# Kernel optimization log

Hardware: AMD Instinct MI355X
Metric: run time of the kernel (lower is better)

Reference implementation:

```python
import jax, jax.numpy as jnp
import numpy as np

EMBED_DIM = 4096
NQ = 32           # query heads
NKV = 8           # kv heads
HEAD = 128        # head dim
KV_SEQ = 4096
B = 8
T = 32
START_POS = 4064  # end_pos = 4096
SCALE = 1.0 / np.sqrt(HEAD)
THETA = 10000.0


def _rope(x, table_len):
    """Faithful replication of the torch module's RoPE, including its bug:
    the torch code unpacks (B,H,T,D)=x.shape on a (B,T_seq,H,D) tensor, so the
    frequency table (of length table_len) is sliced to the first H (=num heads)
    rows and broadcast along the HEAD axis, not the sequence axis.
    x: (B, T_seq, H, D) float32.
    """
    Bn, Tn, H, D = x.shape
    dh = D // 2
    inv_freq = 1.0 / (THETA ** (jnp.arange(dh, dtype=jnp.float32) / dh))  # (dh,)
    pos = jnp.arange(table_len, dtype=jnp.float32)
    freqs = (pos[:, None] * inv_freq[None, :])[:H]  # (H, dh) -- head-indexed!
    cos = jnp.cos(freqs)[None, None]  # (1,1,H,dh)
    sin = jnp.sin(freqs)[None, None]
    xr, xi = x[..., 0::2], x[..., 1::2]  # complex pairs are consecutive elems
    yr = xr * cos - xi * sin
    yi = xr * sin + xi * cos
    return jnp.stack([yr, yi], axis=-1).reshape(Bn, Tn, H, D)


def setup_inputs() -> dict:
    key = jax.random.key(0)
    ks = jax.random.split(key, 5)
    x = jax.random.normal(ks[0], (B, T, EMBED_DIM), dtype=jnp.float32)
    Wq = jax.random.normal(ks[1], (EMBED_DIM, EMBED_DIM), dtype=jnp.float32) * 0.02
    Wk = jax.random.normal(ks[2], (NKV * HEAD, EMBED_DIM), dtype=jnp.float32) * 0.02
    Wv = jax.random.normal(ks[3], (NKV * HEAD, EMBED_DIM), dtype=jnp.float32) * 0.02
    Wo = jax.random.normal(ks[4], (EMBED_DIM, EMBED_DIM), dtype=jnp.float32) * 0.02
    cache_keys = jnp.zeros((B, KV_SEQ * 2, NKV, HEAD), dtype=jnp.float32)
    cache_values = jnp.zeros((B, KV_SEQ * 2, NKV, HEAD), dtype=jnp.float32)
    return {"x": x, "start_pos": START_POS, "cache_keys": cache_keys,
            "cache_values": cache_values, "Wq": Wq, "Wk": Wk, "Wv": Wv, "Wo": Wo}


def reference(x, start_pos, cache_keys, cache_values, Wq, Wk, Wv, Wo):
    Bn, Tn, C = x.shape
    q = (x @ Wq.T).reshape(Bn, Tn, NQ, HEAD)
    k = (x @ Wk.T).reshape(Bn, Tn, NKV, HEAD)
    v = (x @ Wv.T).reshape(Bn, Tn, NKV, HEAD)
    # rope=True branch: q table built for Tn positions, k table for KV_SEQ
    q = _rope(q, Tn)
    k = _rope(k, KV_SEQ)
    end = start_pos + Tn
    # cache write (torch detaches k/v before writing and reads detached views)
    ck = cache_keys.at[:Bn, start_pos:end].set(jax.lax.stop_gradient(k))
    cv = cache_values.at[:Bn, start_pos:end].set(jax.lax.stop_gradient(v))
    k_full = jax.lax.stop_gradient(ck[:Bn, :end])  # (B, end, NKV, D)
    v_full = jax.lax.stop_gradient(cv[:Bn, :end])
    r = NQ // NKV
    kf = jnp.repeat(k_full.transpose(0, 2, 1, 3), r, axis=1)  # (B, NQ, end, D)
    vf = jnp.repeat(v_full.transpose(0, 2, 1, 3), r, axis=1)
    qh = q.transpose(0, 2, 1, 3)                               # (B, NQ, T, D)
    att = jnp.einsum('bhtd,bhsd->bhts', qh, kf) * SCALE        # (B, NQ, T, end)
    causal = jnp.triu(jnp.ones((end, end), dtype=bool), 1)[-Tn:]  # (T, end)
    att = jnp.where(causal[None, None], -jnp.inf, att)
    att = jax.nn.softmax(att, axis=-1)
    out = jnp.einsum('bhts,bhsd->bhtd', att, vf)
    out = out.transpose(0, 2, 1, 3).reshape(Bn, Tn, C)
    return out @ Wo.T
```

## Files before the change

kernel.cpp:

```cpp
#include <hip/hip_runtime.h>
#include <stdint.h>

#define Bb 8
#define Tt 32
#define Ee 4096
#define NQ 32
#define NKV 8
#define HD 128
#define CACHE_S 8192
#define SSPLIT 8
#define SCALE_F 0.08838834764831845f

typedef _Float16 half8 __attribute__((ext_vector_type(8)));
typedef _Float16 half4 __attribute__((ext_vector_type(4)));
typedef float f32x4 __attribute__((ext_vector_type(4)));

static __device__ __forceinline__ _Float16 f2h(float f) { return (_Float16)f; }

__global__ __launch_bounds__(256) void gemm_nt_sk(
    const float* __restrict__ A, const float* __restrict__ W0,
    const float* __restrict__ W1, const float* __restrict__ W2,
    int nsplit1, int nsplit2, float* __restrict__ Cpart, size_t part_stride,
    int K, int Kc, int ldc) {
  __shared__ _Float16 As[64][72];
  __shared__ _Float16 Ws[64][72];
  const int n0 = blockIdx.x * 64;
  const int m0 = blockIdx.y * 64;
  const int kp = blockIdx.z;
  const int kbase = kp * Kc;
  const float* Wp;
  int nr0;
  if (n0 < nsplit1) { Wp = W0; nr0 = n0; }
  else if (n0 < nsplit2) { Wp = W1; nr0 = n0 - nsplit1; }
  else { Wp = W2; nr0 = n0 - nsplit2; }
  const int tid = threadIdx.x;
  const int lane = tid & 63;
  const int wave = tid >> 6;
  const int wm = (wave >> 1) * 32;
  const int wn = (wave & 1) * 32;
  const int l15 = lane & 15;
  const int quad = lane >> 4;
  const int sr = tid >> 4;
  const int sc = (tid & 15) * 4;

  f32x4 acc[2][2];
#pragma unroll
  for (int i = 0; i < 2; i++)
#pragma unroll
    for (int j = 0; j < 2; j++) acc[i][j] = f32x4{0.f, 0.f, 0.f, 0.f};

  float4 pa[4], pw[4];
#pragma unroll
  for (int p = 0; p < 4; p++) {
    const int r = sr + p * 16;
    pa[p] = *(const float4*)&A[(size_t)(m0 + r) * K + kbase + sc];
    pw[p] = *(const float4*)&Wp[(size_t)(nr0 + r) * K + kbase + sc];
  }

  for (int k0 = 0; k0 < Kc; k0 += 64) {
    __syncthreads();
#pragma unroll
    for (int p = 0; p < 4; p++) {
      const int r = sr + p * 16;
      half4 ha = {f2h(pa[p].x), f2h(pa[p].y), f2h(pa[p].z), f2h(pa[p].w)};
      *(half4*)&As[r][sc] = ha;
      half4 hw = {f2h(pw[p].x), f2h(pw[p].y), f2h(pw[p].z), f2h(pw[p].w)};
      *(half4*)&Ws[r][sc] = hw;
    }
    __syncthreads();
    if (k0 + 64 < Kc) {
#pragma unroll
      for (int p = 0; p < 4; p++) {
        const int r = sr + p * 16;
        pa[p] = *(const float4*)&A[(size_t)(m0 + r) * K + kbase + k0 + 64 + sc];
        pw[p] = *(const float4*)&Wp[(size_t)(nr0 + r) * K + kbase + k0 + 64 + sc];
      }
    }
#pragma unroll
    for (int ks = 0; ks < 2; ks++) {
      const int kc = ks * 32 + quad * 8;
      half8 af[2], wf[2];
#pragma unroll
      for (int i = 0; i < 2; i++) {
        af[i] = *(const half8*)&As[wm + i * 16 + l15][kc];
        wf[i] = *(const half8*)&Ws[wn + i * 16 + l15][kc];
      }
#pragma unroll
      for (int i = 0; i < 2; i++)
#pragma unroll
        for (int j = 0; j < 2; j++)
          acc[i][j] = __builtin_amdgcn_mfma_f32_16x16x32_f16(af[i], wf[j],
                                                             acc[i][j], 0, 0, 0);
    }
  }
  float* Cp = Cpart + (size_t)kp * part_stride;
#pragma unroll
  for (int i = 0; i < 2; i++) {
    const int mr = m0 + wm + i * 16 + quad * 4;
#pragma unroll
    for (int j = 0; j < 2; j++) {
      const int nc = n0 + wn + j * 16 + l15;
#pragma unroll
      for (int r = 0; r < 4; r++)
        Cp[(size_t)(mr + r) * ldc + nc] = acc[i][j][r];
    }
  }
}

__global__ __launch_bounds__(256) void rope_scatter(
    const float* __restrict__ qkvp, float* __restrict__ qw,
    float* __restrict__ kw, float* __restrict__ vw) {
  const int pid = blockIdx.x * 256 + threadIdx.x;
  const int m = pid / 3072;
  const int c = pid - m * 3072;
  const int n = c * 2;
  const int b = m >> 5;
  const int t = m & 31;
  const size_t base = (size_t)m * 6144 + n;
  float a0 = 0.f, a1 = 0.f;
#pragma unroll
  for (int p = 0; p < 4; p++) {
    const float2 v = *(const float2*)&qkvp[p * 1572864 + base];
    a0 += v.x;
    a1 += v.y;
  }
  if (n < 4096) {
    const int h = n >> 7;
    const int j = (n & 127) >> 1;
    const float invf = powf(10000.0f, -(float)j * (1.0f / 64.0f));
    float sn, cs;
    sincosf((float)h * invf, &sn, &cs);
    float* dst = qw + ((size_t)(b * NQ + h) * Tt + t) * HD + (j << 1);
    dst[0] = a0 * cs - a1 * sn;
    dst[1] = a0 * sn + a1 * cs;
  } else if (n < 5120) {
    const int nn = n - 4096;
    const int h = nn >> 7;
    const int j = (nn & 127) >> 1;
    const float invf = powf(10000.0f, -(float)j * (1.0f / 64.0f));
    float sn, cs;
    sincosf((float)h * invf, &sn, &cs);
    float* dst = kw + ((size_t)(b * NKV + h) * Tt + t) * HD + (j << 1);
    dst[0] = a0 * cs - a1 * sn;
    dst[1] = a0 * sn + a1 * cs;
  } else {
    const int nn = n - 5120;
    const int h = nn >> 7;
    const int d = nn & 127;
    float* dst = vw + ((size_t)(b * NKV + h) * Tt + t) * HD + d;
    dst[0] = a0;
    dst[1] = a1;
  }
}

__global__ __launch_bounds__(256) void attn_partial(
    const float* __restrict__ qw, const float* __restrict__ kw,
    const float* __restrict__ vw, const float* __restrict__ cacheK,
    const float* __restrict__ cacheV, const int* __restrict__ startp,
    float* __restrict__ pO, float* __restrict__ pM, float* __restrict__ pL) {
  const int blk = blockIdx.x;
  const int split = blk & (SSPLIT - 1);
  const int g = (blk / SSPLIT) & (NKV - 1);
  const int b = blk / (SSPLIT * NKV);
  const int start = *startp;
  const int end = start + Tt;
  int cl = ((end + SSPLIT * 32 - 1) / (SSPLIT * 32)) * 32;
  const int s_begin = split * cl;
  int s_end = s_begin + cl;
  if (s_end > end) s_end = end;

  const int tid = threadIdx.x;
  const int lane = tid & 63;
  const int wave = tid >> 6;
  const int l15 = lane & 15;
  const int quad = lane >> 4;
  const int h = g * 4 + wave;

  __shared__ _Float16 Ks[32][136];
  __shared__ _Float16 Vt[128][40];
  __shared__ _Float16 Ps[4][32][40];

  half8 qf[2][4];
#pragma unroll
  for (int mt = 0; mt < 2; mt++) {
    const int t = mt * 16 + l15;
    const float* qrow = qw + ((size_t)(b * NQ + h) * Tt + t) * HD;
#pragma unroll
    for (int ks = 0; ks < 4; ks++) {
      const int d0 = ks * 32 + quad * 8;
      float4 v0 = *(const float4*)&qrow[d0];
      float4 v1 = *(const float4*)&qrow[d0 + 4];
      half8 hq = {f2h(v0.x), f2h(v0.y), f2h(v0.z), f2h(v0.w),
                  f2h(v1.x), f2h(v1.y), f2h(v1.z), f2h(v1.w)};
      qf[mt][ks] = hq;
    }
  }

  f32x4 Oacc[2][8];
#pragma unroll
  for (int mt = 0; mt < 2; mt++)
#pragma unroll
    for (int dt = 0; dt < 8; dt++) Oacc[mt][dt] = f32x4{0.f, 0.f, 0.f, 0.f};
  float mrow[2][4], lrow[2][4];
#pragma unroll
  for (int mt = 0; mt < 2; mt++)
#pragma unroll
    for (int rr = 0; rr < 4; rr++) { mrow[mt][rr] = -1e30f; lrow[mt][rr] = 0.f; }

  const int str = tid >> 3;
  const int stc = (tid & 7) * 4;

  float4 pk[4], pv[4];
  auto load_chunk = [&](int s0) {
    const int sg = s0 + str;
    const bool valid = sg < end;
    const float* krow;
    const float* vrow;
    if (sg < start) {
      const size_t off = (((size_t)b * CACHE_S + sg) * NKV + g) * HD;
      krow = cacheK + off;
      vrow = cacheV + off;
    } else {
      int loc = sg - start;
      if (loc > Tt - 1) loc = Tt - 1;
      const size_t off = ((size_t)(b * NKV + g) * Tt + loc) * HD;
      krow = kw + off;
      vrow = vw + off;
    }
#pragma unroll
    for (int u = 0; u < 4; u++) {
      const int cc = stc + u * 32;
      pk[u] = valid ? *(const float4*)&krow[cc] : make_float4(0.f, 0.f, 0.f, 0.f);
      pv[u] = valid ? *(const float4*)&vrow[cc] : make_float4(0.f, 0.f, 0.f, 0.f);
    }
  };

  load_chunk(s_begin);

  for (int s0 = s_begin; s0 < s_end; s0 += 32) {
    __syncthreads();
#pragma unroll
    for (int u = 0; u < 4; u++) {
      const int cc = stc + u * 32;
      half4 hk = {f2h(pk[u].x), f2h(pk[u].y), f2h(pk[u].z), f2h(pk[u].w)};
      *(half4*)&Ks[str][cc] = hk;
      Vt[cc + 0][str] = f2h(pv[u].x);
      Vt[cc + 1][str] = f2h(pv[u].y);
      Vt[cc + 2][str] = f2h(pv[u].z);
      Vt[cc + 3][str] = f2h(pv[u].w);
    }
    __syncthreads();
    if (s0 + 32 < s_end) load_chunk(s0 + 32);

    f32x4 st[2][2];
#pragma unroll
    for (int mt = 0; mt < 2; mt++)
#pragma unroll
      for (int nt = 0; nt < 2; nt++) st[mt][nt] = f32x4{0.f, 0.f, 0.f, 0.f};
#pragma unroll
    for (int nt = 0; nt < 2; nt++) {
#pragma unroll
      for (int ks = 0; ks < 4; ks++) {
        half8 kf = *(const half8*)&Ks[nt * 16 + l15][ks * 32 + quad * 8];
        st[0][nt] = __builtin_amdgcn_mfma_f32_16x16x32_f16(qf[0][ks], kf, st[0][nt], 0, 0, 0);
        st[1][nt] = __builtin_amdgcn_mfma_f32_16x16x32_f16(qf[1][ks], kf, st[1][nt], 0, 0, 0);
      }
    }
#pragma unroll
    for (int mt = 0; mt < 2; mt++)
#pragma unroll
      for (int nt = 0; nt < 2; nt++)
#pragma unroll
        for (int rr = 0; rr < 4; rr++) {
          const int t = mt * 16 + quad * 4 + rr;
          const int sg = s0 + nt * 16 + l15;
          const float sv = st[mt][nt][rr] * SCALE_F;
          const bool masked = (sg > start + t) || (sg >= end);
          st[mt][nt][rr] = masked ? -1e30f : sv;
        }
#pragma unroll
    for (int mt = 0; mt < 2; mt++) {
      float rmax[4], rsum[4], al[4];
#pragma unroll
      for (int rr = 0; rr < 4; rr++)
        rmax[rr] = fmaxf(st[mt][0][rr], st[mt][1][rr]);
      for (int mm = 1; mm < 16; mm <<= 1)
#pragma unroll
        for (int rr = 0; rr < 4; rr++)
          rmax[rr] = fmaxf(rmax[rr], __shfl_xor(rmax[rr], mm));
#pragma unroll
      for (int rr = 0; rr < 4; rr++) {
        const float mn = fmaxf(mrow[mt][rr], rmax[rr]);
        al[rr] = __expf(mrow[mt][rr] - mn);
        mrow[mt][rr] = mn;
      }
#pragma unroll
      for (int nt = 0; nt < 2; nt++)
#pragma unroll
        for (int rr = 0; rr < 4; rr++)
          st[mt][nt][rr] = __expf(st[mt][nt][rr] - mrow[mt][rr]);
#pragma unroll
      for (int rr = 0; rr < 4; rr++) rsum[rr] = st[mt][0][rr] + st[mt][1][rr];
      for (int mm = 1; mm < 16; mm <<= 1)
#pragma unroll
        for (int rr = 0; rr < 4; rr++) rsum[rr] += __shfl_xor(rsum[rr], mm);
#pragma unroll
      for (int rr = 0; rr < 4; rr++)
        lrow[mt][rr] = lrow[mt][rr] * al[rr] + rsum[rr];
#pragma unroll
      for (int nt = 0; nt < 2; nt++)
#pragma unroll
        for (int rr = 0; rr < 4; rr++)
          Ps[wave][mt * 16 + quad * 4 + rr][nt * 16 + l15] = f2h(st[mt][nt][rr]);
#pragma unroll
      for (int dt = 0; dt < 8; dt++)
#pragma unroll
        for (int rr = 0; rr < 4; rr++) Oacc[mt][dt][rr] *= al[rr];
    }
    half8 pf0 = *(const half8*)&Ps[wave][l15][quad * 8];
    half8 pf1 = *(const half8*)&Ps[wave][16 + l15][quad * 8];
#pragma unroll
    for (int dt = 0; dt < 8; dt++) {
      half8 vf = *(const half8*)&Vt[dt * 16 + l15][quad * 8];
      Oacc[0][dt] = __builtin_amdgcn_mfma_f32_16x16x32_f16(pf0, vf, Oacc[0][dt], 0, 0, 0);
      Oacc[1][dt] = __builtin_amdgcn_mfma_f32_16x16x32_f16(pf1, vf, Oacc[1][dt], 0, 0, 0);
    }
  }

  const size_t rowbase = (size_t)(b * NQ + h) * Tt;
#pragma unroll
  for (int mt = 0; mt < 2; mt++)
#pragma unroll
    for (int rr = 0; rr < 4; rr++) {
      const int t = mt * 16 + quad * 4 + rr;
      const size_t pbase = ((rowbase + t) * SSPLIT + split) * (size_t)HD;
#pragma unroll
      for (int dt = 0; dt < 8; dt++)
        pO[pbase + dt * 16 + l15] = Oacc[mt][dt][rr];
      if (l15 == 0) {
        pM[(rowbase + t) * SSPLIT + split] = mrow[mt][rr];
        pL[(rowbase + t) * SSPLIT + split] = lrow[mt][rr];
      }
    }
}

__global__ __launch_bounds__(128) void attn_combine(
    const float* __restrict__ pO, const float* __restrict__ pM,
    const float* __restrict__ pL, float* __restrict__ att) {
  const int row = blockIdx.x;
  const int d = threadIdx.x;
  float m[SSPLIT], l[SSPLIT];
  float ms = -3.0e30f;
#pragma unroll
  for (int i = 0; i < SSPLIT; i++) {
    m[i] = pM[row * SSPLIT + i];
    l[i] = pL[row * SSPLIT + i];
    ms = fmaxf(ms, m[i]);
  }
  float ls = 0.f, o = 0.f;
#pragma unroll
  for (int i = 0; i < SSPLIT; i++) {
    const float w = __expf(m[i] - ms);
    ls += l[i] * w;
    o += pO[((size_t)row * SSPLIT + i) * HD + d] * w;
  }
  o /= fmaxf(ls, 1e-30f);
  const int b = row / (NQ * Tt);
  const int hh = (row / Tt) % NQ;
  const int t = row % Tt;
  att[((size_t)(b * Tt + t)) * Ee + hh * HD + d] = o;
}

__global__ __launch_bounds__(256) void reduce2(const float* __restrict__ p0,
                                               const float* __restrict__ p1,
                                               float* __restrict__ out) {
  const int i = (blockIdx.x * 256 + threadIdx.x) * 4;
  float4 a = *(const float4*)&p0[i];
  float4 b = *(const float4*)&p1[i];
  float4 r = make_float4(a.x + b.x, a.y + b.y, a.z + b.z, a.w + b.w);
  *(float4*)&out[i] = r;
}

extern "C" void kernel_launch(void* const* d_in, const int* in_sizes, int n_in,
                              void* d_out, int out_size, void* d_ws,
                              size_t ws_size, hipStream_t stream) {
  const float* x = (const float*)d_in[0];
  const int* startp = (const int*)d_in[1];
  const float* cacheK = (const float*)d_in[2];
  const float* cacheV = (const float*)d_in[3];
  const float* Wq = (const float*)d_in[4];
  const float* Wk = (const float*)d_in[5];
  const float* Wv = (const float*)d_in[6];
  const float* Wo = (const float*)d_in[7];
  float* out = (float*)d_out;
  float* ws = (float*)d_ws;

  float* qkvp = ws;
  float* pO = qkvp + 6291456;
  float* qw = pO + 8388608;
  float* kw = qw + 1048576;
  float* vw = kw + 262144;
  float* pM = vw + 262144;
  float* pL = pM + 65536;
  float* att = pL + 65536;
  float* woP = att + 1048576;

  const dim3 blk(256);
  gemm_nt_sk<<<dim3(96, 4, 4), blk, 0, stream>>>(
      x, Wq, Wk, Wv, 4096, 5120, qkvp, (size_t)256 * 6144, 4096, 1024, 6144);
  rope_scatter<<<dim3(3072), blk, 0, stream>>>(qkvp, qw, kw, vw);
  attn_partial<<<dim3(Bb * NKV * SSPLIT), blk, 0, stream>>>(
      qw, kw, vw, cacheK, cacheV, startp, pO, pM, pL);
  attn_combine<<<dim3(Bb * NQ * Tt), dim3(128), 0, stream>>>(pO, pM, pL, att);
  gemm_nt_sk<<<dim3(64, 4, 2), blk, 0, stream>>>(
      att, Wo, Wo, Wo, 4096, 4096, woP, (size_t)256 * 4096, 4096, 2048, 4096);
  reduce2<<<dim3(1024), blk, 0, stream>>>(woP, woP + 1048576, out);
}
```

Measured before the change: 652.9 us.

## Double-buffer KV chunk prefetch in attention and split Wo GEMM K four ways

The attention partial kernel now keeps two register buffers of K/V data, so loads for chunks two steps ahead are issued before the current chunk is computed. The Q fragment load is moved after the first prefetches so they overlap. This is meant to hide global-memory latency, at the cost of more registers. Separately, the output projection GEMM now splits K four ways instead of two, giving 1024 blocks for better CU occupancy, and a reduce4 kernel sums the four partials, which adds partial-buffer traffic.

```diff
diff --git a/kernel.cpp b/kernel.cpp
--- a/kernel.cpp
+++ b/kernel.cpp
@@ -180,38 +180,11 @@
   __shared__ _Float16 Vt[128][40];
   __shared__ _Float16 Ps[4][32][40];
 
-  half8 qf[2][4];
-#pragma unroll
-  for (int mt = 0; mt < 2; mt++) {
-    const int t = mt * 16 + l15;
-    const float* qrow = qw + ((size_t)(b * NQ + h) * Tt + t) * HD;
-#pragma unroll
-    for (int ks = 0; ks < 4; ks++) {
-      const int d0 = ks * 32 + quad * 8;
-      float4 v0 = *(const float4*)&qrow[d0];
-      float4 v1 = *(const float4*)&qrow[d0 + 4];
-      half8 hq = {f2h(v0.x), f2h(v0.y), f2h(v0.z), f2h(v0.w),
-                  f2h(v1.x), f2h(v1.y), f2h(v1.z), f2h(v1.w)};
-      qf[mt][ks] = hq;
-    }
-  }
-
-  f32x4 Oacc[2][8];
-#pragma unroll
-  for (int mt = 0; mt < 2; mt++)
-#pragma unroll
-    for (int dt = 0; dt < 8; dt++) Oacc[mt][dt] = f32x4{0.f, 0.f, 0.f, 0.f};
-  float mrow[2][4], lrow[2][4];
-#pragma unroll
-  for (int mt = 0; mt < 2; mt++)
-#pragma unroll
-    for (int rr = 0; rr < 4; rr++) { mrow[mt][rr] = -1e30f; lrow[mt][rr] = 0.f; }
-
   const int str = tid >> 3;
   const int stc = (tid & 7) * 4;
 
-  float4 pk[4], pv[4];
-  auto load_chunk = [&](int s0) {
+  float4 pkA[4], pvA[4], pkB[4], pvB[4];
+  auto load_chunk = [&](int s0, float4* pk, float4* pv) {
     const int sg = s0 + str;
     const bool valid = sg < end;
     const float* krow;
@@ -234,11 +207,7 @@
       pv[u] = valid ? *(const float4*)&vrow[cc] : make_float4(0.f, 0.f, 0.f, 0.f);
     }
   };
-
-  load_chunk(s_begin);
-
-  for (int s0 = s_begin; s0 < s_end; s0 += 32) {
-    __syncthreads();
+  auto commit_chunk = [&](const float4* pk, const float4* pv) {
 #pragma unroll
     for (int u = 0; u < 4; u++) {
       const int cc = stc + u * 32;
@@ -249,9 +218,39 @@
       Vt[cc + 2][str] = f2h(pv[u].z);
       Vt[cc + 3][str] = f2h(pv[u].w);
     }
-    __syncthreads();
-    if (s0 + 32 < s_end) load_chunk(s0 + 32);
-
+  };
+
+  load_chunk(s_begin, pkA, pvA);
+  if (s_begin + 32 < s_end) load_chunk(s_begin + 32, pkB, pvB);
+
+  half8 qf[2][4];
+#pragma unroll
+  for (int mt = 0; mt < 2; mt++) {
+    const int t = mt * 16 + l15;
+    const float* qrow = qw + ((size_t)(b * NQ + h) * Tt + t) * HD;
+#pragma unroll
+    for (int ks = 0; ks < 4; ks++) {
+      const int d0 = ks * 32 + quad * 8;
+      float4 v0 = *(const float4*)&qrow[d0];
+      float4 v1 = *(const float4*)&qrow[d0 + 4];
+      half8 hq = {f2h(v0.x), f2h(v0.y), f2h(v0.z), f2h(v0.w),
+                  f2h(v1.x), f2h(v1.y), f2h(v1.z), f2h(v1.w)};
+      qf[mt][ks] = hq;
+    }
+  }
+
+  f32x4 Oacc[2][8];
+#pragma unroll
+  for (int mt = 0; mt < 2; mt++)
+#pragma unroll
+    for (int dt = 0; dt < 8; dt++) Oacc[mt][dt] = f32x4{0.f, 0.f, 0.f, 0.f};
+  float mrow[2][4], lrow[2][4];
+#pragma unroll
+  for (int mt = 0; mt < 2; mt++)
+#pragma unroll
+    for (int rr = 0; rr < 4; rr++) { mrow[mt][rr] = -1e30f; lrow[mt][rr] = 0.f; }
+
+  auto compute_chunk = [&](int s0) {
     f32x4 st[2][2];
 #pragma unroll
     for (int mt = 0; mt < 2; mt++)
@@ -325,6 +324,21 @@
       Oacc[0][dt] = __builtin_amdgcn_mfma_f32_16x16x32_f16(pf0, vf, Oacc[0][dt], 0, 0, 0);
       Oacc[1][dt] = __builtin_amdgcn_mfma_f32_16x16x32_f16(pf1, vf, Oacc[1][dt], 0, 0, 0);
     }
+  };
+
+  for (int s0 = s_begin; s0 < s_end; s0 += 64) {
+    __syncthreads();
+    commit_chunk(pkA, pvA);
+    __syncthreads();
+    if (s0 + 64 < s_end) load_chunk(s0 + 64, pkA, pvA);
+    compute_chunk(s0);
+    if (s0 + 32 < s_end) {
+      __syncthreads();
+      commit_chunk(pkB, pvB);
+      __syncthreads();
+      if (s0 + 96 < s_end) load_chunk(s0 + 96, pkB, pvB);
+      compute_chunk(s0 + 32);
+    }
   }
 
   const size_t rowbase = (size_t)(b * NQ + h) * Tt;
@@ -371,13 +385,15 @@
   att[((size_t)(b * Tt + t)) * Ee + hh * HD + d] = o;
 }
 
-__global__ __launch_bounds__(256) void reduce2(const float* __restrict__ p0,
-                                               const float* __restrict__ p1,
+__global__ __launch_bounds__(256) void reduce4(const float* __restrict__ p,
                                                float* __restrict__ out) {
   const int i = (blockIdx.x * 256 + threadIdx.x) * 4;
-  float4 a = *(const float4*)&p0[i];
-  float4 b = *(const float4*)&p1[i];
-  float4 r = make_float4(a.x + b.x, a.y + b.y, a.z + b.z, a.w + b.w);
+  float4 a = *(const float4*)&p[i];
+  float4 b = *(const float4*)&p[i + 1048576];
+  float4 c = *(const float4*)&p[i + 2097152];
+  float4 d = *(const float4*)&p[i + 3145728];
+  float4 r = make_float4(a.x + b.x + c.x + d.x, a.y + b.y + c.y + d.y,
+                         a.z + b.z + c.z + d.z, a.w + b.w + c.w + d.w);
   *(float4*)&out[i] = r;
 }
 
@@ -412,7 +428,7 @@
   attn_partial<<<dim3(Bb * NKV * SSPLIT), blk, 0, stream>>>(
       qw, kw, vw, cacheK, cacheV, startp, pO, pM, pL);
   attn_combine<<<dim3(Bb * NQ * Tt), dim3(128), 0, stream>>>(pO, pM, pL, att);
-  gemm_nt_sk<<<dim3(64, 4, 2), blk, 0, stream>>>(
-      att, Wo, Wo, Wo, 4096, 4096, woP, (size_t)256 * 4096, 4096, 2048, 4096);
-  reduce2<<<dim3(1024), blk, 0, stream>>>(woP, woP + 1048576, out);
-}
+  gemm_nt_sk<<<dim3(64, 4, 4), blk, 0, stream>>>(
+      att, Wo, Wo, Wo, 4096, 4096, woP, (size_t)256 * 4096, 4096, 1024, 4096);
+  reduce4<<<dim3(1024), blk, 0, stream>>>(woP, out);
+}
```

New measurement: 668.0 us. 1.02x slower.
